# Kernel tuning notes

Hardware: AMD Instinct MI355X
Metric: run time of the kernel (lower is better)

## Reference

```python
import jax, jax.numpy as jnp
import numpy as np

B, S, QD, KD, VD, OD = 8, 2048, 768, 768, 768, 512

def setup_inputs() -> dict:
    key = jax.random.key(0)
    ks = jax.random.split(key, 14)
    s_q = 1.0 / np.sqrt(QD)
    s_k = 1.0 / np.sqrt(KD)
    s_v = 1.0 / np.sqrt(VD)
    return {
        "query": jax.random.normal(ks[0], (B, S, QD), jnp.float32),
        "key": jax.random.normal(ks[1], (B, S, KD), jnp.float32),
        "value": jax.random.normal(ks[2], (B, S, VD), jnp.float32),
        "Wqr": jax.random.normal(ks[3], (QD, OD), jnp.float32) * s_q,
        "bqr": jnp.zeros((OD,), jnp.float32),
        "Wqi": jax.random.normal(ks[4], (QD, OD), jnp.float32) * s_q,
        "bqi": jnp.zeros((OD,), jnp.float32),
        "Wkr": jax.random.normal(ks[5], (KD, OD), jnp.float32) * s_k,
        "bkr": jnp.zeros((OD,), jnp.float32),
        "Wki": jax.random.normal(ks[6], (KD, OD), jnp.float32) * s_k,
        "bki": jnp.zeros((OD,), jnp.float32),
        "Wv": jax.random.normal(ks[7], (VD, OD), jnp.float32) * s_v,
        "bv": jnp.zeros((OD,), jnp.float32),
        "coherence_weight": jnp.asarray(1.0, jnp.float32),
    }

def reference(query, key, value, Wqr, bqr, Wqi, bqi, Wkr, bkr, Wki, bki, Wv, bv, coherence_weight):
    # Complex-valued projections (real/imag parts via separate linears)
    q_r = jnp.einsum("bsq,qo->bso", query, Wqr) + bqr
    q_i = jnp.einsum("bsq,qo->bso", query, Wqi) + bqi
    k_r = jnp.einsum("bsk,ko->bso", key, Wkr) + bkr
    k_i = jnp.einsum("bsk,ko->bso", key, Wki) + bki
    v = jnp.einsum("bsv,vo->bso", value, Wv) + bv
    # Complex QK^T: (q_r + i q_i)(k_r - i k_i)^T pieces, as in the torch code
    att_real = jnp.einsum("bso,bto->bst", q_r, k_r) + jnp.einsum("bso,bto->bst", q_i, k_i)
    att_imag = jnp.einsum("bso,bto->bst", q_i, k_r) - jnp.einsum("bso,bto->bst", q_r, k_i)
    att_mag = jnp.sqrt(att_real ** 2 + att_imag ** 2)
    scale = jnp.asarray(1.0 / np.sqrt(OD), att_mag.dtype)
    weights = jax.nn.softmax(att_mag * scale, axis=-1)  # [B,S,S]
    output = jnp.einsum("bst,bto->bso", weights, v)  # [B,S,OD]
    coherence = jnp.mean(att_imag ** 2) * coherence_weight
    return output, coherence
```

## Files before the change

kernel.cpp:

```cpp
#include <hip/hip_runtime.h>
#include <math.h>
#include <stdint.h>

#define S_    2048
#define SCALE_ 0.044194173824159216f

typedef __attribute__((ext_vector_type(8))) short short8;
typedef __attribute__((ext_vector_type(4))) float f32x4;

#define MFMA16(a, b, c) __builtin_amdgcn_mfma_f32_16x16x32_bf16((a), (b), (c), 0, 0, 0)

__device__ __forceinline__ void glds16(const void* g, void* l) {
  __builtin_amdgcn_global_load_lds(
      (const __attribute__((address_space(1))) void*)g,
      (__attribute__((address_space(3))) void*)l, 16, 0, 0);
}

__device__ __forceinline__ unsigned short f2bf(float f) {
  unsigned u = __float_as_uint(f);
  u += 0x7FFFu + ((u >> 16) & 1u);
  return (unsigned short)(u >> 16);
}

__global__ __launch_bounds__(256) void convert3_kernel(
    const float* __restrict__ a, const float* __restrict__ b,
    const float* __restrict__ c, unsigned short* __restrict__ oa,
    unsigned short* __restrict__ ob, unsigned short* __restrict__ oc) {
  int i = blockIdx.x * 256 + threadIdx.x;
  int which = i / 3145728;
  int off = i - which * 3145728;
  const float* s = (which == 0) ? a : (which == 1) ? b : c;
  unsigned short* d = (which == 0) ? oa : (which == 1) ? ob : oc;
  float4 v = ((const float4*)s)[off];
  ushort4 o;
  o.x = f2bf(v.x); o.y = f2bf(v.y); o.z = f2bf(v.z); o.w = f2bf(v.w);
  ((ushort4*)d)[off] = o;
}

__global__ void init_fused_kernel(const float* __restrict__ bqr,
                                  const float* __restrict__ bqi,
                                  const float* __restrict__ bkr,
                                  const float* __restrict__ bki,
                                  const float* __restrict__ bv, float* bq,
                                  float* bk, float* bvo, float* lsum,
                                  float* coh) {
  int t = blockIdx.x * 256 + threadIdx.x;
  if (t < 512) { bq[t] = bqr[t]; bk[t] = bkr[t]; bvo[t] = bv[t]; }
  else if (t < 1024) { bq[t] = bqi[t - 512]; bk[t] = bki[t - 512]; }
  if (t < 16384) lsum[t] = 0.f;
  if (t == 0) *coh = 0.f;
}

__global__ __launch_bounds__(256) void wtrans_all_kernel(
    const float* __restrict__ Wqr, const float* __restrict__ Wqi,
    const float* __restrict__ Wkr, const float* __restrict__ Wki,
    const float* __restrict__ Wv, unsigned short* __restrict__ WTQ,
    unsigned short* __restrict__ WTK, unsigned short* __restrict__ WTV) {
  __shared__ float t[32][33];
  const float* W;
  unsigned short* Wt;
  int row_off;
  switch (blockIdx.z) {
    case 0: W = Wqr; Wt = WTQ; row_off = 0; break;
    case 1: W = Wqi; Wt = WTQ; row_off = 512; break;
    case 2: W = Wkr; Wt = WTK; row_off = 0; break;
    case 3: W = Wki; Wt = WTK; row_off = 512; break;
    default: W = Wv; Wt = WTV; row_off = 0; break;
  }
  int n0 = blockIdx.x * 32, k0 = blockIdx.y * 32;
  int tx = threadIdx.x & 31, ty = threadIdx.x >> 5;
#pragma unroll
  for (int r = 0; r < 4; ++r)
    t[ty + r * 8][tx] = W[(size_t)(k0 + ty + r * 8) * 512 + n0 + tx];
  __syncthreads();
#pragma unroll
  for (int r = 0; r < 4; ++r)
    Wt[(size_t)(row_off + n0 + ty + r * 8) * 768 + k0 + tx] =
        f2bf(t[tx][ty + r * 8]);
}

__global__ __launch_bounds__(256, 2) void proj_fused_kernel(
    const unsigned short* __restrict__ XQ, const unsigned short* __restrict__ XK,
    const unsigned short* __restrict__ XV, const unsigned short* __restrict__ WTQ,
    const unsigned short* __restrict__ WTK, const unsigned short* __restrict__ WTV,
    const float* __restrict__ BQ, const float* __restrict__ BK,
    const float* __restrict__ BV, unsigned short* __restrict__ QCAT,
    unsigned short* __restrict__ KCAT, unsigned short* __restrict__ VT) {
  __shared__ char lds[65536];
  const int tid = threadIdx.x;
  const int lane = tid & 63, wid = tid >> 6;
  const int wi = wid >> 1, wj = wid & 1;

  const unsigned short* Xb;
  const unsigned short* Wt;
  const float* bias;
  unsigned short* Y;
  int N, vt_mode, bx = blockIdx.x;
  if (bx < 8)       { Xb = XQ; Wt = WTQ; bias = BQ; Y = QCAT; N = 1024; vt_mode = 0; }
  else if (bx < 16) { Xb = XK; Wt = WTK; bias = BK; Y = KCAT; N = 1024; vt_mode = 0; bx -= 8; }
  else              { Xb = XV; Wt = WTV; bias = BV; Y = VT;   N = 512;  vt_mode = 1; bx -= 16; }

  const int m0 = blockIdx.y * 128, n0 = bx * 128;
  const char* Xc = (const char*)Xb;
  const char* Wc = (const char*)Wt;
  const int tile = wid >> 1;

  const char* sp[8];
  int sd[8];
#pragma unroll
  for (int iss = 0; iss < 8; ++iss) {
    int gbase = wid * 512 + iss * 64;
    int loc = (gbase & 1023) + lane;
    int r = loc >> 3, blk = loc & 7;
    int sb = blk ^ (r & 7);
    sp[iss] = (tile == 0) ? Xc + (size_t)(m0 + r) * 1536 + sb * 16
                          : Wc + (size_t)(n0 + r) * 1536 + sb * 16;
    sd[iss] = gbase * 16;
  }

  f32x4 acc[4][4] = {};

#pragma unroll
  for (int iss = 0; iss < 8; ++iss) glds16(sp[iss], lds + sd[iss]);

  for (int s = 0; s < 12; ++s) {
    __syncthreads();
    if (s + 1 < 12) {
      char* wb = lds + ((s + 1) & 1) * 32768;
#pragma unroll
      for (int iss = 0; iss < 8; ++iss)
        glds16(sp[iss] + (s + 1) * 128, wb + sd[iss]);
    }
    const char* rb = lds + (s & 1) * 32768;
#pragma unroll
    for (int kk = 0; kk < 2; ++kk) {
      int blk = kk * 4 + (lane >> 4);
      short8 a[4];
#pragma unroll
      for (int i = 0; i < 4; ++i) {
        int row = wi * 64 + i * 16 + (lane & 15);
        a[i] = *(const short8*)(rb + row * 128 + ((blk ^ (row & 7)) << 4));
      }
#pragma unroll
      for (int j = 0; j < 4; ++j) {
        int row = wj * 64 + j * 16 + (lane & 15);
        short8 b = *(const short8*)(rb + 16384 + row * 128 +
                                    ((blk ^ (row & 7)) << 4));
#pragma unroll
        for (int i = 0; i < 4; ++i) acc[i][j] = MFMA16(a[i], b, acc[i][j]);
      }
    }
  }

#pragma unroll
  for (int j = 0; j < 4; ++j) {
    int n = n0 + wj * 64 + j * 16 + (lane & 15);
    float bn = bias[n];
    if (!vt_mode) {
#pragma unroll
      for (int i = 0; i < 4; ++i) {
        int mrow = m0 + wi * 64 + i * 16 + (lane >> 4) * 4;
#pragma unroll
        for (int r = 0; r < 4; ++r)
          Y[(size_t)(mrow + r) * N + n] = f2bf(acc[i][j][r] + bn);
      }
    } else {
#pragma unroll
      for (int i = 0; i < 4; ++i) {
        int mrow = m0 + wi * 64 + i * 16 + (lane >> 4) * 4;
        int b = mrow >> 11, key = mrow & 2047;
        ushort4 o;
        o.x = f2bf(acc[i][j][0] + bn);
        o.y = f2bf(acc[i][j][1] + bn);
        o.z = f2bf(acc[i][j][2] + bn);
        o.w = f2bf(acc[i][j][3] + bn);
        *(ushort4*)&Y[((size_t)b * 512 + n) * 2048 + key] = o;
      }
    }
  }
}

__global__ __launch_bounds__(256, 3) void score_kernel(
    const unsigned short* __restrict__ Qcat,
    const unsigned short* __restrict__ Kcat, unsigned short* __restrict__ P,
    float* __restrict__ lsum, float* __restrict__ coh) {
  __shared__ char lds[49152];
  const int tid = threadIdx.x;
  const int lane = tid & 63, wid = tid >> 6;
  const int wm = wid >> 1;
  const int wn = wid & 1;
  const int lr = lane & 15;
  const int lk = lane >> 4;
  const int l8 = lane >> 3, lb = lane & 7;

  const int id = blockIdx.x;
  const int batch = id & 7;
  const int tile = id >> 3;
  const int q0 = (tile >> 5) << 7;
  const int k0 = (tile & 31) << 6;

  const char* Qc = (const char*)Qcat + ((size_t)batch * 2048 + q0) * 2048;
  const char* Kc = (const char*)Kcat + ((size_t)batch * 2048 + k0) * 2048;

  const char* sp[6];
  int sd[6];
#pragma unroll
  for (int u = 0; u < 6; ++u) {
    int L = wid * 6 + u;
    int row = (L < 16) ? ((L << 3) + l8) : (((L - 16) << 3) + l8);
    int sb = lb ^ (row & 7);
    const char* base = (L < 16) ? Qc : Kc;
    sp[u] = base + (size_t)row * 2048 + (sb & 3) * 16 + (sb >> 2) * 1024;
    sd[u] = L << 10;
  }

  int aoff_lo[4], aoff_hi[4], boff_lo[2], boff_hi[2];
#pragma unroll
  for (int i = 0; i < 4; ++i) {
    int ar = wm * 64 + i * 16 + lr;
    aoff_lo[i] = ar * 128 + ((lk ^ (ar & 7)) << 4);
    aoff_hi[i] = ar * 128 + (((4 + lk) ^ (ar & 7)) << 4);
  }
#pragma unroll
  for (int j = 0; j < 2; ++j) {
    int br = wn * 32 + j * 16 + lr;
    boff_lo[j] = 16384 + br * 128 + ((lk ^ (br & 7)) << 4);
    boff_hi[j] = 16384 + br * 128 + (((4 + lk) ^ (br & 7)) << 4);
  }

  f32x4 accre[4][2] = {}, accim[4][2] = {};
  const short sg = (short)0x8000;
  const short8 SGN = {sg, sg, sg, sg, sg, sg, sg, sg};

#pragma unroll
  for (int u = 0; u < 6; ++u) glds16(sp[u], lds + sd[u]);

  for (int t = 0; t < 16; ++t) {
    __syncthreads();
    if (t + 1 < 16) {
      char* wb = lds + ((t + 1) & 1) * 24576;
#pragma unroll
      for (int u = 0; u < 6; ++u) glds16(sp[u] + (t + 1) * 64, wb + sd[u]);
    }
    const char* rb = lds + (t & 1) * 24576;
    short8 alo[4], ahi[4];
#pragma unroll
    for (int i = 0; i < 4; ++i) {
      alo[i] = *(const short8*)(rb + aoff_lo[i]);
      ahi[i] = *(const short8*)(rb + aoff_hi[i]);
    }
#pragma unroll
    for (int j = 0; j < 2; ++j) {
      short8 blo = *(const short8*)(rb + boff_lo[j]);
      short8 bhi = *(const short8*)(rb + boff_hi[j]);
      short8 bhin = bhi ^ SGN;
#pragma unroll
      for (int i = 0; i < 4; ++i) {
        accre[i][j] = MFMA16(alo[i], blo, accre[i][j]);
        accre[i][j] = MFMA16(ahi[i], bhi, accre[i][j]);
        accim[i][j] = MFMA16(ahi[i], blo, accim[i][j]);
        accim[i][j] = MFMA16(alo[i], bhin, accim[i][j]);
      }
    }
  }

  float csum = 0.f;
  size_t prow_base = (size_t)batch * 2048;
#pragma unroll
  for (int i = 0; i < 4; ++i) {
#pragma unroll
    for (int r = 0; r < 4; ++r) {
      int row = q0 + wm * 64 + i * 16 + lk * 4 + r;
      unsigned short* prow = P + (prow_base + row) * 2048;
      float rs = 0.f;
#pragma unroll
      for (int j = 0; j < 2; ++j) {
        float re = accre[i][j][r], im = accim[i][j][r];
        csum += im * im;
        float p = __expf(sqrtf(re * re + im * im) * SCALE_);
        rs += p;
        prow[k0 + wn * 32 + j * 16 + lr] = f2bf(p);
      }
      rs += __shfl_xor(rs, 1, 64);
      rs += __shfl_xor(rs, 2, 64);
      rs += __shfl_xor(rs, 4, 64);
      rs += __shfl_xor(rs, 8, 64);
      if (lr == 0) atomicAdd(&lsum[prow_base + row], rs);
    }
  }
#pragma unroll
  for (int m = 1; m < 64; m <<= 1) csum += __shfl_xor(csum, m, 64);
  float* cred = (float*)lds;
  __syncthreads();
  if (lane == 0) cred[wid] = csum;
  __syncthreads();
  if (tid == 0) atomicAdd(coh, cred[0] + cred[1] + cred[2] + cred[3]);
}

__global__ __launch_bounds__(256, 2) void pv_kernel(
    const unsigned short* __restrict__ P, const unsigned short* __restrict__ Vt,
    const float* __restrict__ lsum, float* __restrict__ out) {
  __shared__ char lds[65536];
  const int tid = threadIdx.x;
  const int lane = tid & 63, wid = tid >> 6;
  const int wi = wid >> 1, wj = wid & 1;

  int id = blockIdx.x;
  int w = (id & 7) * 64 + (id >> 3);
  int batch = w >> 6, tilein = w & 63;
  int i0 = (tilein >> 2) * 128;
  int o0 = (tilein & 3) * 128;

  const char* Pc = (const char*)P + (size_t)batch * 2048 * 4096;
  const char* Vc = (const char*)Vt + (size_t)batch * 512 * 4096;
  const int tile = wid >> 1;

  const char* sp[8];
  int sd[8];
#pragma unroll
  for (int iss = 0; iss < 8; ++iss) {
    int gbase = wid * 512 + iss * 64;
    int loc = (gbase & 1023) + lane;
    int r = loc >> 3, blk = loc & 7;
    int sb = blk ^ (r & 7);
    sp[iss] = (tile == 0) ? Pc + (size_t)(i0 + r) * 4096 + sb * 16
                          : Vc + (size_t)(o0 + r) * 4096 + sb * 16;
    sd[iss] = gbase * 16;
  }

  f32x4 acc[4][4] = {};

#pragma unroll
  for (int iss = 0; iss < 8; ++iss) glds16(sp[iss], lds + sd[iss]);

  for (int s = 0; s < 32; ++s) {
    __syncthreads();
    if (s + 1 < 32) {
      char* wb = lds + ((s + 1) & 1) * 32768;
#pragma unroll
      for (int iss = 0; iss < 8; ++iss)
        glds16(sp[iss] + (s + 1) * 128, wb + sd[iss]);
    }
    const char* rb = lds + (s & 1) * 32768;
#pragma unroll
    for (int kk = 0; kk < 2; ++kk) {
      int blk = kk * 4 + (lane >> 4);
      short8 a[4];
#pragma unroll
      for (int i = 0; i < 4; ++i) {
        int row = wi * 64 + i * 16 + (lane & 15);
        a[i] = *(const short8*)(rb + row * 128 + ((blk ^ (row & 7)) << 4));
      }
#pragma unroll
      for (int j = 0; j < 4; ++j) {
        int row = wj * 64 + j * 16 + (lane & 15);
        short8 b = *(const short8*)(rb + 16384 + row * 128 +
                                    ((blk ^ (row & 7)) << 4));
#pragma unroll
        for (int i = 0; i < 4; ++i) acc[i][j] = MFMA16(a[i], b, acc[i][j]);
      }
    }
  }

#pragma unroll
  for (int i = 0; i < 4; ++i) {
    int mrow = i0 + wi * 64 + i * 16 + (lane >> 4) * 4;
    float linv[4];
#pragma unroll
    for (int r = 0; r < 4; ++r)
      linv[r] = 1.0f / lsum[(size_t)batch * 2048 + mrow + r];
#pragma unroll
    for (int j = 0; j < 4; ++j) {
      int n = o0 + wj * 64 + j * 16 + (lane & 15);
#pragma unroll
      for (int r = 0; r < 4; ++r)
        out[((size_t)batch * 2048 + mrow + r) * 512 + n] = acc[i][j][r] * linv[r];
    }
  }
}

__global__ void finalize_kernel(const float* __restrict__ coh,
                                const float* __restrict__ cw,
                                float* __restrict__ out_last) {
  *out_last = (*coh) * (1.0f / 33554432.0f) * (*cw);
}

extern "C" void kernel_launch(void* const* d_in, const int* in_sizes, int n_in,
                              void* d_out, int out_size, void* d_ws,
                              size_t ws_size, hipStream_t stream) {
  const float* query = (const float*)d_in[0];
  const float* key   = (const float*)d_in[1];
  const float* value = (const float*)d_in[2];
  const float* Wqr = (const float*)d_in[3];
  const float* bqr = (const float*)d_in[4];
  const float* Wqi = (const float*)d_in[5];
  const float* bqi = (const float*)d_in[6];
  const float* Wkr = (const float*)d_in[7];
  const float* bkr = (const float*)d_in[8];
  const float* Wki = (const float*)d_in[9];
  const float* bki = (const float*)d_in[10];
  const float* Wv  = (const float*)d_in[11];
  const float* bv  = (const float*)d_in[12];
  const float* cw  = (const float*)d_in[13];
  float* out = (float*)d_out;

  char* ws = (char*)d_ws;
  unsigned short* XQ   = (unsigned short*)(ws + 0);
  unsigned short* XK   = (unsigned short*)(ws + 25165824);
  unsigned short* XV   = (unsigned short*)(ws + 50331648);
  unsigned short* Pbuf = (unsigned short*)(ws + 0);
  unsigned short* WTQ  = (unsigned short*)(ws + 75497472);
  unsigned short* WTK  = (unsigned short*)(ws + 77070336);
  unsigned short* WTV  = (unsigned short*)(ws + 78643200);
  float* BQ   = (float*)(ws + 79429632);
  float* BK   = (float*)(ws + 79433728);
  float* BV   = (float*)(ws + 79437824);
  unsigned short* QCAT = (unsigned short*)(ws + 79441920);
  unsigned short* KCAT = (unsigned short*)(ws + 112996352);
  unsigned short* VT   = (unsigned short*)(ws + 146550784);
  float* LSUM = (float*)(ws + 163328000);
  float* COH  = (float*)(ws + 163393536);
  if (ws_size < 163393600) return;

  convert3_kernel<<<36864, 256, 0, stream>>>(query, key, value, XQ, XK, XV);
  init_fused_kernel<<<64, 256, 0, stream>>>(bqr, bqi, bkr, bki, bv, BQ, BK, BV,
                                            LSUM, COH);
  wtrans_all_kernel<<<dim3(16, 24, 5), 256, 0, stream>>>(Wqr, Wqi, Wkr, Wki, Wv,
                                                         WTQ, WTK, WTV);

  proj_fused_kernel<<<dim3(20, 128), 256, 0, stream>>>(
      XQ, XK, XV, WTQ, WTK, WTV, BQ, BK, BV, QCAT, KCAT, VT);

  score_kernel<<<4096, 256, 0, stream>>>(QCAT, KCAT, Pbuf, LSUM, COH);
  pv_kernel<<<512, 256, 0, stream>>>(Pbuf, VT, LSUM, out);
  finalize_kernel<<<1, 1, 0, stream>>>(COH, cw, out + 8388608);
}
```

Measured before the change: 371.1 us.

## Enlarge score tile to 256x128 with 512 threads and triple-buffered LDS pipeline

```diff
diff --git a/kernel.cpp b/kernel.cpp
--- a/kernel.cpp
+++ b/kernel.cpp
@@ -180,11 +180,11 @@
   }
 }
 
-__global__ __launch_bounds__(256, 3) void score_kernel(
+__global__ __launch_bounds__(512, 2) void score_kernel(
     const unsigned short* __restrict__ Qcat,
     const unsigned short* __restrict__ Kcat, unsigned short* __restrict__ P,
     float* __restrict__ lsum, float* __restrict__ coh) {
-  __shared__ char lds[49152];
+  __shared__ char lds[147456];
   const int tid = threadIdx.x;
   const int lane = tid & 63, wid = tid >> 6;
   const int wm = wid >> 1;
@@ -196,8 +196,8 @@
   const int id = blockIdx.x;
   const int batch = id & 7;
   const int tile = id >> 3;
-  const int q0 = (tile >> 5) << 7;
-  const int k0 = (tile & 31) << 6;
+  const int q0 = (tile >> 4) << 8;
+  const int k0 = (tile & 15) << 7;
 
   const char* Qc = (const char*)Qcat + ((size_t)batch * 2048 + q0) * 2048;
   const char* Kc = (const char*)Kcat + ((size_t)batch * 2048 + k0) * 2048;
@@ -207,14 +207,14 @@
 #pragma unroll
   for (int u = 0; u < 6; ++u) {
     int L = wid * 6 + u;
-    int row = (L < 16) ? ((L << 3) + l8) : (((L - 16) << 3) + l8);
+    int row = ((L & 31) << 3) + l8;
     int sb = lb ^ (row & 7);
-    const char* base = (L < 16) ? Qc : Kc;
+    const char* base = (L < 32) ? Qc : Kc;
     sp[u] = base + (size_t)row * 2048 + (sb & 3) * 16 + (sb >> 2) * 1024;
     sd[u] = L << 10;
   }
 
-  int aoff_lo[4], aoff_hi[4], boff_lo[2], boff_hi[2];
+  int aoff_lo[4], aoff_hi[4], boff_lo[4], boff_hi[4];
 #pragma unroll
   for (int i = 0; i < 4; ++i) {
     int ar = wm * 64 + i * 16 + lr;
@@ -222,37 +222,49 @@
     aoff_hi[i] = ar * 128 + (((4 + lk) ^ (ar & 7)) << 4);
   }
 #pragma unroll
-  for (int j = 0; j < 2; ++j) {
-    int br = wn * 32 + j * 16 + lr;
-    boff_lo[j] = 16384 + br * 128 + ((lk ^ (br & 7)) << 4);
-    boff_hi[j] = 16384 + br * 128 + (((4 + lk) ^ (br & 7)) << 4);
-  }
-
-  f32x4 accre[4][2] = {}, accim[4][2] = {};
+  for (int j = 0; j < 4; ++j) {
+    int br = wn * 64 + j * 16 + lr;
+    boff_lo[j] = 32768 + br * 128 + ((lk ^ (br & 7)) << 4);
+    boff_hi[j] = 32768 + br * 128 + (((4 + lk) ^ (br & 7)) << 4);
+  }
+
+  f32x4 accre[4][4] = {}, accim[4][4] = {};
   const short sg = (short)0x8000;
   const short8 SGN = {sg, sg, sg, sg, sg, sg, sg, sg};
 
 #pragma unroll
   for (int u = 0; u < 6; ++u) glds16(sp[u], lds + sd[u]);
+#pragma unroll
+  for (int u = 0; u < 6; ++u) glds16(sp[u] + 64, lds + 49152 + sd[u]);
+  asm volatile("s_waitcnt vmcnt(6)" ::: "memory");
+  __builtin_amdgcn_s_barrier();
 
   for (int t = 0; t < 16; ++t) {
-    __syncthreads();
-    if (t + 1 < 16) {
-      char* wb = lds + ((t + 1) & 1) * 24576;
-#pragma unroll
-      for (int u = 0; u < 6; ++u) glds16(sp[u] + (t + 1) * 64, wb + sd[u]);
-    }
-    const char* rb = lds + (t & 1) * 24576;
+    const char* rb = lds + (t % 3) * 49152;
+    char* wb = lds + ((t + 2) % 3) * 49152;
+    const bool pre = (t < 14);
     short8 alo[4], ahi[4];
 #pragma unroll
-    for (int i = 0; i < 4; ++i) {
-      alo[i] = *(const short8*)(rb + aoff_lo[i]);
-      ahi[i] = *(const short8*)(rb + aoff_hi[i]);
-    }
-#pragma unroll
-    for (int j = 0; j < 2; ++j) {
+    for (int j = 0; j < 4; ++j) {
+      if (j == 0) {
+#pragma unroll
+        for (int i = 0; i < 4; ++i) {
+          alo[i] = *(const short8*)(rb + aoff_lo[i]);
+          ahi[i] = *(const short8*)(rb + aoff_hi[i]);
+        }
+      }
       short8 blo = *(const short8*)(rb + boff_lo[j]);
       short8 bhi = *(const short8*)(rb + boff_hi[j]);
+      if (pre) {
+        if (j == 0)      { glds16(sp[0] + (t + 2) * 64, wb + sd[0]);
+                           glds16(sp[1] + (t + 2) * 64, wb + sd[1]); }
+        else if (j == 1) { glds16(sp[2] + (t + 2) * 64, wb + sd[2]);
+                           glds16(sp[3] + (t + 2) * 64, wb + sd[3]); }
+        else if (j == 2) { glds16(sp[4] + (t + 2) * 64, wb + sd[4]); }
+        else             { glds16(sp[5] + (t + 2) * 64, wb + sd[5]); }
+      }
+      __builtin_amdgcn_s_barrier();
+      __builtin_amdgcn_s_setprio(1);
       short8 bhin = bhi ^ SGN;
 #pragma unroll
       for (int i = 0; i < 4; ++i) {
@@ -261,8 +273,15 @@
         accim[i][j] = MFMA16(ahi[i], blo, accim[i][j]);
         accim[i][j] = MFMA16(alo[i], bhin, accim[i][j]);
       }
-    }
-  }
+      __builtin_amdgcn_s_setprio(0);
+      if (j == 3) {
+        if (t < 14)       asm volatile("s_waitcnt vmcnt(6)" ::: "memory");
+        else if (t == 14) asm volatile("s_waitcnt vmcnt(0)" ::: "memory");
+      }
+      __builtin_amdgcn_s_barrier();
+    }
+  }
+  __syncthreads();
 
   float csum = 0.f;
   size_t prow_base = (size_t)batch * 2048;
@@ -274,12 +293,12 @@
       unsigned short* prow = P + (prow_base + row) * 2048;
       float rs = 0.f;
 #pragma unroll
-      for (int j = 0; j < 2; ++j) {
+      for (int j = 0; j < 4; ++j) {
         float re = accre[i][j][r], im = accim[i][j][r];
         csum += im * im;
         float p = __expf(sqrtf(re * re + im * im) * SCALE_);
         rs += p;
-        prow[k0 + wn * 32 + j * 16 + lr] = f2bf(p);
+        prow[k0 + wn * 64 + j * 16 + lr] = f2bf(p);
       }
       rs += __shfl_xor(rs, 1, 64);
       rs += __shfl_xor(rs, 2, 64);
@@ -291,10 +310,14 @@
 #pragma unroll
   for (int m = 1; m < 64; m <<= 1) csum += __shfl_xor(csum, m, 64);
   float* cred = (float*)lds;
-  __syncthreads();
   if (lane == 0) cred[wid] = csum;
   __syncthreads();
-  if (tid == 0) atomicAdd(coh, cred[0] + cred[1] + cred[2] + cred[3]);
+  if (tid == 0) {
+    float s = 0.f;
+#pragma unroll
+    for (int w = 0; w < 8; ++w) s += cred[w];
+    atomicAdd(coh, s);
+  }
 }
 
 __global__ __launch_bounds__(256, 2) void pv_kernel(
@@ -431,7 +454,7 @@
   proj_fused_kernel<<<dim3(20, 128), 256, 0, stream>>>(
       XQ, XK, XV, WTQ, WTK, WTV, BQ, BK, BV, QCAT, KCAT, VT);
 
-  score_kernel<<<4096, 256, 0, stream>>>(QCAT, KCAT, Pbuf, LSUM, COH);
+  score_kernel<<<1024, 512, 0, stream>>>(QCAT, KCAT, Pbuf, LSUM, COH);
   pv_kernel<<<512, 256, 0, stream>>>(Pbuf, VT, LSUM, out);
   finalize_kernel<<<1, 1, 0, stream>>>(COH, cw, out + 8388608);
 }
```

Result: faster. 358.1 us (-3.5%).
